# Kernel optimization log

Hardware: AMD Instinct MI355X
Metric: run time of the kernel (lower is better)

Reference implementation:

```python
import jax, jax.numpy as jnp
import numpy as np

NUM_GRAPHS = 2048
D_IN, D_H1, D_H2 = 1536, 64, 32


def setup_inputs() -> dict:
    key = jax.random.key(0)
    ks = jax.random.split(key, 8)
    features = jax.random.normal(ks[0], (131072, D_IN), dtype=jnp.float32)
    batch = jnp.sort(jax.random.randint(ks[1], (131072,), 0, NUM_GRAPHS, dtype=jnp.int64))
    # MLP params (Linear: y = x @ W.T + b), kaiming-ish scale
    W1 = jax.random.normal(ks[2], (D_H1, D_IN), dtype=jnp.float32) * (1.0 / np.sqrt(D_IN))
    b1 = jnp.zeros((D_H1,), dtype=jnp.float32)
    W2 = jax.random.normal(ks[3], (D_H2, D_H1), dtype=jnp.float32) * (1.0 / np.sqrt(D_H1))
    b2 = jnp.zeros((D_H2,), dtype=jnp.float32)
    W3 = jax.random.normal(ks[4], (1, D_H2), dtype=jnp.float32) * (1.0 / np.sqrt(D_H2))
    b3 = jnp.zeros((1,), dtype=jnp.float32)
    return {"features": features, "batch": batch, "W1": W1, "b1": b1,
            "W2": W2, "b2": b2, "W3": W3, "b3": b3}


def reference(features, batch, W1, b1, W2, b2, W3, b3):
    # Vectorized per-graph mean pooling (empty graphs -> zero features,
    # matching the torch branch that feeds zeros to the classifier).
    sums = jax.ops.segment_sum(features, batch, num_segments=NUM_GRAPHS)  # [G, D]
    counts = jax.ops.segment_sum(jnp.ones((features.shape[0],), features.dtype),
                                 batch, num_segments=NUM_GRAPHS)          # [G]
    means = sums / jnp.maximum(counts, 1.0)[:, None]                      # [G, D]
    # Tiny MLP classifier (dropout is identity in eval mode)
    h = jax.nn.relu(means @ W1.T + b1)
    h = jax.nn.relu(h @ W2.T + b2)
    out = h @ W3.T + b3                                                   # [G, 1]
    return out[:, 0]                                                      # [G]
```

## Files before the change

kernel.cpp:

```cpp
#include <hip/hip_runtime.h>

#define NGRAPHS 2048
#define DIN     1536
#define DH1     64
#define DH2     32
#define POOL_BLOCKS 1280

typedef float fvec4 __attribute__((ext_vector_type(4)));

__global__ void find_offsets_kernel(const int* __restrict__ batch, int n,
                                    int* __restrict__ offsets,
                                    int* __restrict__ counter) {
    int i = blockIdx.x * blockDim.x + threadIdx.x;
    if (i == 0) *counter = 0;
    if (i >= n) return;
    int b = batch[i];
    int prev = (i == 0) ? -1 : batch[i - 1];
    for (int g = prev + 1; g <= b; ++g) offsets[g] = i;
    if (i == n - 1) {
        for (int g = b + 1; g <= NGRAPHS; ++g) offsets[g] = n;
    }
}

__global__ __launch_bounds__(384) void pool_mlp_ws_kernel(
    const float* __restrict__ features,
    const int* __restrict__ offsets,
    const float* __restrict__ W1, const float* __restrict__ b1,
    const float* __restrict__ W2, const float* __restrict__ b2,
    const float* __restrict__ W3, const float* __restrict__ b3,
    float* __restrict__ out,
    int* __restrict__ counter)
{
    const int tid  = threadIdx.x;
    const int lane = tid & 63;
    const int wave = tid >> 6;

    __shared__ float mean_s[DIN];
    __shared__ float h1_s[DH1];
    __shared__ float h2_s[DH2];
    __shared__ int   g_s;

    const fvec4* __restrict__ F4 = reinterpret_cast<const fvec4*>(features);

    for (;;) {
        if (tid == 0) g_s = atomicAdd(counter, 1);
        __syncthreads();
        const int g = g_s;
        if (g >= NGRAPHS) break;

        const int s = offsets[g];
        const int e = offsets[g + 1];

        fvec4 a0 = (fvec4)(0.f);
        fvec4 a1 = (fvec4)(0.f);
        fvec4 a2 = (fvec4)(0.f);
        fvec4 a3 = (fvec4)(0.f);
        int r = s;
        for (; r + 4 <= e; r += 4) {
            fvec4 v0 = __builtin_nontemporal_load(&F4[(size_t)(r + 0) * (DIN / 4) + tid]);
            fvec4 v1 = __builtin_nontemporal_load(&F4[(size_t)(r + 1) * (DIN / 4) + tid]);
            fvec4 v2 = __builtin_nontemporal_load(&F4[(size_t)(r + 2) * (DIN / 4) + tid]);
            fvec4 v3 = __builtin_nontemporal_load(&F4[(size_t)(r + 3) * (DIN / 4) + tid]);
            a0 += v0; a1 += v1; a2 += v2; a3 += v3;
        }
        for (; r < e; ++r) {
            fvec4 v = __builtin_nontemporal_load(&F4[(size_t)r * (DIN / 4) + tid]);
            a0 += v;
        }
        a0 += a1 + a2 + a3;

        const int cnt = e - s;
        const float inv = 1.0f / (float)(cnt > 1 ? cnt : 1);
        a0 *= inv;
        reinterpret_cast<fvec4*>(mean_s)[tid] = a0;
        __syncthreads();

        const fvec4* __restrict__ m4 = reinterpret_cast<const fvec4*>(mean_s);
        for (int j = wave; j < DH1; j += 6) {
            const fvec4* __restrict__ w4 =
                reinterpret_cast<const fvec4*>(W1 + (size_t)j * DIN);
            float acc = 0.f;
            #pragma unroll
            for (int k = 0; k < DIN / 4 / 64; ++k) {
                fvec4 w = w4[k * 64 + lane];
                fvec4 m = m4[k * 64 + lane];
                acc += m.x * w.x + m.y * w.y + m.z * w.z + m.w * w.w;
            }
            #pragma unroll
            for (int off = 32; off; off >>= 1) acc += __shfl_xor(acc, off, 64);
            if (lane == 0) h1_s[j] = fmaxf(acc + b1[j], 0.f);
        }
        __syncthreads();

        for (int j = wave; j < DH2; j += 6) {
            float acc = h1_s[lane] * W2[(size_t)j * DH1 + lane];
            #pragma unroll
            for (int off = 32; off; off >>= 1) acc += __shfl_xor(acc, off, 64);
            if (lane == 0) h2_s[j] = fmaxf(acc + b2[j], 0.f);
        }
        __syncthreads();

        if (wave == 0) {
            float acc = (lane < DH2) ? h2_s[lane] * W3[lane] : 0.f;
            #pragma unroll
            for (int off = 32; off; off >>= 1) acc += __shfl_xor(acc, off, 64);
            if (lane == 0) out[g] = acc + b3[0];
        }
        __syncthreads();
    }
}

extern "C" void kernel_launch(void* const* d_in, const int* in_sizes, int n_in,
                              void* d_out, int out_size, void* d_ws, size_t ws_size,
                              hipStream_t stream) {
    const float* features = (const float*)d_in[0];
    const int*   batch    = (const int*)d_in[1];
    const float* W1 = (const float*)d_in[2];
    const float* b1 = (const float*)d_in[3];
    const float* W2 = (const float*)d_in[4];
    const float* b2 = (const float*)d_in[5];
    const float* W3 = (const float*)d_in[6];
    const float* b3 = (const float*)d_in[7];
    float* out = (float*)d_out;

    const int n = in_sizes[1];
    int* counter = (int*)d_ws;
    int* offsets = (int*)d_ws + 64;

    find_offsets_kernel<<<(n + 255) / 256, 256, 0, stream>>>(batch, n, offsets,
                                                             counter);
    pool_mlp_ws_kernel<<<POOL_BLOCKS, 384, 0, stream>>>(features, offsets,
                                                        W1, b1, W2, b2, W3, b3,
                                                        out, counter);
}
```

Before: 163.4 us.

## Software-pipeline graph pooling with the previous graph's MLP layer-one compute

Restructures the persistent work-stealing kernel into a two-stage pipeline. Each block double-buffers the mean vector, so the feature-row loads for the next graph are interleaved with the W1 dot products of the current graph, and the atomic fetch for the graph after that is issued early. The aim is to hide the MLP compute and barrier latency behind the memory-bound pooling stream, at the cost of more registers, predicated loads and doubled shared memory. The grid also shrinks from 1280 to 768 blocks.

```diff
diff --git a/kernel.cpp b/kernel.cpp
--- a/kernel.cpp
+++ b/kernel.cpp
@@ -4,7 +4,7 @@
 #define DIN     1536
 #define DH1     64
 #define DH2     32
-#define POOL_BLOCKS 1280
+#define BLOCKS  768
 
 typedef float fvec4 __attribute__((ext_vector_type(4)));
 
@@ -22,7 +22,7 @@
     }
 }
 
-__global__ __launch_bounds__(384) void pool_mlp_ws_kernel(
+__global__ __launch_bounds__(384) void pool_mlp_pipe_kernel(
     const float* __restrict__ features,
     const int* __restrict__ offsets,
     const float* __restrict__ W1, const float* __restrict__ b1,
@@ -35,78 +35,104 @@
     const int lane = tid & 63;
     const int wave = tid >> 6;
 
-    __shared__ float mean_s[DIN];
+    __shared__ float mean_s[2][DIN];
     __shared__ float h1_s[DH1];
     __shared__ float h2_s[DH2];
-    __shared__ int   g_s;
+    __shared__ int   next_s;
 
     const fvec4* __restrict__ F4 = reinterpret_cast<const fvec4*>(features);
 
-    for (;;) {
-        if (tid == 0) g_s = atomicAdd(counter, 1);
-        __syncthreads();
-        const int g = g_s;
-        if (g >= NGRAPHS) break;
+    if (tid == 0) next_s = atomicAdd(counter, 1);
+    __syncthreads();
+    int g_nxt = next_s;
+    int g_cur = NGRAPHS;
+    int cb = 0;
 
-        const int s = offsets[g];
-        const int e = offsets[g + 1];
+    while (g_cur < NGRAPHS || g_nxt < NGRAPHS) {
+        if (tid == 0) {
+            int f = (g_nxt < NGRAPHS) ? atomicAdd(counter, 1) : NGRAPHS;
+            next_s = f;
+        }
+        const int nb = cb ^ 1;
 
-        fvec4 a0 = (fvec4)(0.f);
-        fvec4 a1 = (fvec4)(0.f);
-        fvec4 a2 = (fvec4)(0.f);
-        fvec4 a3 = (fvec4)(0.f);
-        int r = s;
-        for (; r + 4 <= e; r += 4) {
-            fvec4 v0 = __builtin_nontemporal_load(&F4[(size_t)(r + 0) * (DIN / 4) + tid]);
-            fvec4 v1 = __builtin_nontemporal_load(&F4[(size_t)(r + 1) * (DIN / 4) + tid]);
-            fvec4 v2 = __builtin_nontemporal_load(&F4[(size_t)(r + 2) * (DIN / 4) + tid]);
-            fvec4 v3 = __builtin_nontemporal_load(&F4[(size_t)(r + 3) * (DIN / 4) + tid]);
-            a0 += v0; a1 += v1; a2 += v2; a3 += v3;
+        int s2 = 0, e2 = 0;
+        if (g_nxt < NGRAPHS) { s2 = offsets[g_nxt]; e2 = offsets[g_nxt + 1]; }
+        int r = s2;
+        fvec4 acc0 = (fvec4)(0.f), acc1 = (fvec4)(0.f);
+
+        if (g_cur < NGRAPHS) {
+            const fvec4* __restrict__ m4 =
+                reinterpret_cast<const fvec4*>(mean_s[cb]);
+            for (int jj = 0; jj < 11; ++jj) {
+                const int j = wave + 6 * jj;
+                fvec4 v0 = (fvec4)(0.f), v1 = (fvec4)(0.f), v2 = (fvec4)(0.f);
+                fvec4 v3 = (fvec4)(0.f), v4 = (fvec4)(0.f), v5 = (fvec4)(0.f);
+                if (r + 0 < e2) v0 = __builtin_nontemporal_load(&F4[(size_t)(r + 0) * (DIN / 4) + tid]);
+                if (r + 1 < e2) v1 = __builtin_nontemporal_load(&F4[(size_t)(r + 1) * (DIN / 4) + tid]);
+                if (r + 2 < e2) v2 = __builtin_nontemporal_load(&F4[(size_t)(r + 2) * (DIN / 4) + tid]);
+                if (r + 3 < e2) v3 = __builtin_nontemporal_load(&F4[(size_t)(r + 3) * (DIN / 4) + tid]);
+                if (r + 4 < e2) v4 = __builtin_nontemporal_load(&F4[(size_t)(r + 4) * (DIN / 4) + tid]);
+                if (r + 5 < e2) v5 = __builtin_nontemporal_load(&F4[(size_t)(r + 5) * (DIN / 4) + tid]);
+                int ladv = e2 - r; ladv = (ladv < 0) ? 0 : (ladv > 6 ? 6 : ladv);
+                r += ladv;
+
+                if (j < DH1) {
+                    const fvec4* __restrict__ w4 =
+                        reinterpret_cast<const fvec4*>(W1 + (size_t)j * DIN);
+                    float d = 0.f;
+                    #pragma unroll
+                    for (int k = 0; k < 6; ++k) {
+                        fvec4 w = w4[k * 64 + lane];
+                        fvec4 m = m4[k * 64 + lane];
+                        d += m.x * w.x + m.y * w.y + m.z * w.z + m.w * w.w;
+                    }
+                    #pragma unroll
+                    for (int off = 32; off; off >>= 1) d += __shfl_xor(d, off, 64);
+                    if (lane == 0) h1_s[j] = fmaxf(d + b1[j], 0.f);
+                }
+                acc0 += v0 + v2 + v4;
+                acc1 += v1 + v3 + v5;
+            }
         }
-        for (; r < e; ++r) {
-            fvec4 v = __builtin_nontemporal_load(&F4[(size_t)r * (DIN / 4) + tid]);
-            a0 += v;
+        for (; r + 4 <= e2; r += 4) {
+            fvec4 u0 = __builtin_nontemporal_load(&F4[(size_t)(r + 0) * (DIN / 4) + tid]);
+            fvec4 u1 = __builtin_nontemporal_load(&F4[(size_t)(r + 1) * (DIN / 4) + tid]);
+            fvec4 u2 = __builtin_nontemporal_load(&F4[(size_t)(r + 2) * (DIN / 4) + tid]);
+            fvec4 u3 = __builtin_nontemporal_load(&F4[(size_t)(r + 3) * (DIN / 4) + tid]);
+            acc0 += u0 + u2;
+            acc1 += u1 + u3;
         }
-        a0 += a1 + a2 + a3;
+        for (; r < e2; ++r)
+            acc0 += __builtin_nontemporal_load(&F4[(size_t)r * (DIN / 4) + tid]);
 
-        const int cnt = e - s;
-        const float inv = 1.0f / (float)(cnt > 1 ? cnt : 1);
-        a0 *= inv;
-        reinterpret_cast<fvec4*>(mean_s)[tid] = a0;
-        __syncthreads();
-
-        const fvec4* __restrict__ m4 = reinterpret_cast<const fvec4*>(mean_s);
-        for (int j = wave; j < DH1; j += 6) {
-            const fvec4* __restrict__ w4 =
-                reinterpret_cast<const fvec4*>(W1 + (size_t)j * DIN);
-            float acc = 0.f;
-            #pragma unroll
-            for (int k = 0; k < DIN / 4 / 64; ++k) {
-                fvec4 w = w4[k * 64 + lane];
-                fvec4 m = m4[k * 64 + lane];
-                acc += m.x * w.x + m.y * w.y + m.z * w.z + m.w * w.w;
-            }
-            #pragma unroll
-            for (int off = 32; off; off >>= 1) acc += __shfl_xor(acc, off, 64);
-            if (lane == 0) h1_s[j] = fmaxf(acc + b1[j], 0.f);
+        if (g_nxt < NGRAPHS) {
+            const int cnt = e2 - s2;
+            const float inv = 1.0f / (float)(cnt > 1 ? cnt : 1);
+            fvec4 mm = (acc0 + acc1) * inv;
+            reinterpret_cast<fvec4*>(mean_s[nb])[tid] = mm;
         }
         __syncthreads();
+        const int g_fut = next_s;
 
-        for (int j = wave; j < DH2; j += 6) {
-            float acc = h1_s[lane] * W2[(size_t)j * DH1 + lane];
-            #pragma unroll
-            for (int off = 32; off; off >>= 1) acc += __shfl_xor(acc, off, 64);
-            if (lane == 0) h2_s[j] = fmaxf(acc + b2[j], 0.f);
+        if (g_cur < NGRAPHS) {
+            for (int j = wave; j < DH2; j += 6) {
+                float a = h1_s[lane] * W2[(size_t)j * DH1 + lane];
+                #pragma unroll
+                for (int off = 32; off; off >>= 1) a += __shfl_xor(a, off, 64);
+                if (lane == 0) h2_s[j] = fmaxf(a + b2[j], 0.f);
+            }
         }
         __syncthreads();
+        if (g_cur < NGRAPHS && wave == 0) {
+            float a = (lane < DH2) ? h2_s[lane] * W3[lane] : 0.f;
+            #pragma unroll
+            for (int off = 32; off; off >>= 1) a += __shfl_xor(a, off, 64);
+            if (lane == 0) out[g_cur] = a + b3[0];
+        }
 
-        if (wave == 0) {
-            float acc = (lane < DH2) ? h2_s[lane] * W3[lane] : 0.f;
-            #pragma unroll
-            for (int off = 32; off; off >>= 1) acc += __shfl_xor(acc, off, 64);
-            if (lane == 0) out[g] = acc + b3[0];
-        }
-        __syncthreads();
+        g_cur = g_nxt;
+        g_nxt = g_fut;
+        cb = nb;
     }
 }
 
@@ -129,7 +155,7 @@
 
     find_offsets_kernel<<<(n + 255) / 256, 256, 0, stream>>>(batch, n, offsets,
                                                              counter);
-    pool_mlp_ws_kernel<<<POOL_BLOCKS, 384, 0, stream>>>(features, offsets,
-                                                        W1, b1, W2, b2, W3, b3,
-                                                        out, counter);
+    pool_mlp_pipe_kernel<<<BLOCKS, 384, 0, stream>>>(features, offsets,
+                                                     W1, b1, W2, b2, W3, b3,
+                                                     out, counter);
 }
```

Result: slower. 174.5 us (+6.8%).
